# Kernel optimization log

Hardware: AMD Instinct MI355X
Metric: run time of the kernel (lower is better)

Reference implementation:

```python
import jax, jax.numpy as jnp
import numpy as np
import math

B, N, M, O = 64, 2048, 64, 128  # batch, neurons, in_dims, out_dims


def setup_inputs() -> dict:
    key = jax.random.key(0)
    kx, kw, kb = jax.random.split(key, 3)
    s = 1.0 / math.sqrt(M + O)
    x = jax.random.normal(kx, (B, N, M), dtype=jnp.float32)
    # master weights fp32, init U(-s, s) as in the torch module
    w1 = jax.random.uniform(kw, (M, O, N), dtype=jnp.float32, minval=-s, maxval=s)
    b1 = jnp.zeros((1, N, O), dtype=jnp.float32)
    return {"x": x, "w1": w1, "b1": b1}


def reference(x, w1, b1):
    # N independent per-neuron linears: [B,N,M] x [M,O,N] -> [B,N,O]
    # cast master weights/bias to compute dtype (matches .to(x.dtype))
    w = w1.astype(x.dtype)
    b = b1.astype(x.dtype)
    return jnp.einsum('bnm,mon->bno', x, w) + b
```

## Files before the change

### kernel.cpp

```cpp
#include <hip/hip_runtime.h>
#include <hip/hip_bf16.h>

#define N_TOT 2048
#define M_DIM 64
#define O_DIM 128
#define NT 8

typedef __bf16 bf16x8 __attribute__((ext_vector_type(8)));
typedef float f32x4 __attribute__((ext_vector_type(4)));

__global__ __launch_bounds__(512, 2) void superlinear_mfma(
    const float* __restrict__ x, const float* __restrict__ w1,
    const float* __restrict__ b1, float* __restrict__ out)
{
    __shared__ unsigned char wlds[3 * NT * 32 * M_DIM * 2];

    const int tid  = threadIdx.x;
    const int lane = tid & 63;
    const int wave = tid >> 6;

    const int bid  = blockIdx.x;
    const int nblk = (bid & 7) * 32 + (bid >> 3);
    const int n0   = nblk * NT;
    const int n    = n0 + wave;

    const int col = lane & 15;
    const int kg  = lane >> 4;

    const int half = tid & 1;
    const int ol   = (tid >> 1) & 31;
    const int mseg = tid >> 6;

    const size_t MSTR = (size_t)O_DIM * N_TOT;

    auto stage_issue = [&](int c, float4* r) {
        const float* gp = w1 + ((size_t)(mseg * 8) * O_DIM + (c * 32 + ol)) * N_TOT
                             + n0 + half * 4;
        #pragma unroll
        for (int mm = 0; mm < 8; ++mm)
            r[mm] = *(const float4*)(gp + (size_t)mm * MSTR);
    };
    auto stage_write = [&](int c, const float4* r) {
        unsigned base = (unsigned)(c % 3) * 32768u;
        #pragma unroll
        for (int j = 0; j < 4; ++j) {
            int nn = half * 4 + j;
            bf16x8 v;
            #pragma unroll
            for (int mm = 0; mm < 8; ++mm)
                v[mm] = (__bf16)(((const float*)&r[mm])[j]);
            unsigned addr = (unsigned)(nn * 4096 + ol * 128 + mseg * 16);
            addr ^= (unsigned)((ol & 7) << 4);
            *(bf16x8*)(wlds + base + addr) = v;
        }
    };

    float4 srA[8], srB[8];
    stage_issue(0, srA);

    float4 xr[2][4][2];
    #pragma unroll
    for (int kc = 0; kc < 2; ++kc)
        #pragma unroll
        for (int bt = 0; bt < 4; ++bt) {
            int b = bt * 16 + col;
            const float* xp = x + ((size_t)b * N_TOT + n) * M_DIM + kc * 32 + kg * 8;
            xr[kc][bt][0] = *(const float4*)xp;
            xr[kc][bt][1] = *(const float4*)(xp + 4);
        }
    float bv[8];
    #pragma unroll
    for (int ot = 0; ot < 8; ++ot)
        bv[ot] = b1[(size_t)n * O_DIM + ot * 16 + col];

    stage_issue(1, srB);

    stage_write(0, srA);

    bf16x8 af[2][4];
    #pragma unroll
    for (int kc = 0; kc < 2; ++kc)
        #pragma unroll
        for (int bt = 0; bt < 4; ++bt) {
            const float* lp = (const float*)&xr[kc][bt][0];
            const float* hp = (const float*)&xr[kc][bt][1];
            bf16x8 v;
            #pragma unroll
            for (int j = 0; j < 4; ++j) {
                v[j]     = (__bf16)lp[j];
                v[4 + j] = (__bf16)hp[j];
            }
            af[kc][bt] = v;
        }

    asm volatile("s_waitcnt lgkmcnt(0)" ::: "memory");
    __builtin_amdgcn_s_barrier();
    __builtin_amdgcn_sched_barrier(0);

    const unsigned sw = (unsigned)(col & 7) << 4;
    #pragma unroll
    for (int c = 0; c < 4; ++c) {
        if (c < 2) stage_issue(c + 2, (c & 1) ? srB : srA);

        unsigned base = (unsigned)(c % 3) * 32768u;
        f32x4 acc[4][2];
        #pragma unroll
        for (int otl = 0; otl < 2; ++otl) {
            unsigned la = (unsigned)(wave * 4096 + otl * 2048 + col * 128 + kg * 16);
            bf16x8 bf0 = *(const bf16x8*)(wlds + base + (la ^ sw));
            bf16x8 bf1 = *(const bf16x8*)(wlds + base + ((la + 64) ^ sw));
            f32x4 ci;
            float b0 = bv[c * 2 + otl];
            ci[0] = b0; ci[1] = b0; ci[2] = b0; ci[3] = b0;
            #pragma unroll
            for (int bt = 0; bt < 4; ++bt) {
                acc[bt][otl] = __builtin_amdgcn_mfma_f32_16x16x32_bf16(af[0][bt], bf0, ci,           0, 0, 0);
                acc[bt][otl] = __builtin_amdgcn_mfma_f32_16x16x32_bf16(af[1][bt], bf1, acc[bt][otl], 0, 0, 0);
            }
        }

        if (c < 3) stage_write(c + 1, (c & 1) ? srA : srB);

        #pragma unroll
        for (int bt = 0; bt < 4; ++bt)
            #pragma unroll
            for (int r = 0; r < 4; ++r) {
                int b = bt * 16 + kg * 4 + r;
                float* op = out + ((size_t)b * N_TOT + n) * O_DIM + c * 32 + col;
                op[0]  = acc[bt][0][r];
                op[16] = acc[bt][1][r];
            }

        if (c < 3) {
            asm volatile("s_waitcnt lgkmcnt(0)" ::: "memory");
            __builtin_amdgcn_s_barrier();
            __builtin_amdgcn_sched_barrier(0);
        }
    }
}

extern "C" void kernel_launch(void* const* d_in, const int* in_sizes, int n_in,
                              void* d_out, int out_size, void* d_ws, size_t ws_size,
                              hipStream_t stream) {
    const float* x  = (const float*)d_in[0];
    const float* w1 = (const float*)d_in[1];
    const float* b1 = (const float*)d_in[2];
    float* out = (float*)d_out;
    superlinear_mfma<<<dim3(256), dim3(512), 0, stream>>>(x, w1, b1, out);
}
```

Before: 35.42 us.

## Split output dim across blocks; use 1024 smaller blocks with single-stage LDS

Restructures the grid so each block handles 8 neurons and a 32-wide slice of the output dimension, launching 1024 blocks of 256 threads instead of 256 blocks of 512. The weight slice is staged into LDS once, which removes the triple-buffered per-chunk pipeline and the barriers inside the loop. Each wave now covers two neurons and iterates over batch tiles, prefetching the next x tile while it computes. The aim is more blocks for occupancy and load balance and less synchronisation, at the cost of re-reading x four times (once per output slice) and losing the overlap of weight loads with compute.

```diff
diff --git a/kernel.cpp b/kernel.cpp
--- a/kernel.cpp
+++ b/kernel.cpp
@@ -5,24 +5,27 @@
 #define M_DIM 64
 #define O_DIM 128
 #define NT 8
+#define OC 32
 
 typedef __bf16 bf16x8 __attribute__((ext_vector_type(8)));
 typedef float f32x4 __attribute__((ext_vector_type(4)));
 
-__global__ __launch_bounds__(512, 2) void superlinear_mfma(
+__global__ __launch_bounds__(256, 4) void superlinear_mfma(
     const float* __restrict__ x, const float* __restrict__ w1,
     const float* __restrict__ b1, float* __restrict__ out)
 {
-    __shared__ unsigned char wlds[3 * NT * 32 * M_DIM * 2];
+    __shared__ unsigned char wlds[NT * OC * M_DIM * 2];
 
     const int tid  = threadIdx.x;
     const int lane = tid & 63;
     const int wave = tid >> 6;
 
-    const int bid  = blockIdx.x;
-    const int nblk = (bid & 7) * 32 + (bid >> 3);
-    const int n0   = nblk * NT;
-    const int n    = n0 + wave;
+    const int bid = blockIdx.x;
+    const int swz = (bid & 7) * 128 + (bid >> 3);
+    const int nq  = swz >> 2;
+    const int oq  = swz & 3;
+    const int n0  = nq * NT;
+    const int o0  = oq * OC;
 
     const int col = lane & 15;
     const int kg  = lane >> 4;
@@ -33,108 +36,97 @@
 
     const size_t MSTR = (size_t)O_DIM * N_TOT;
 
-    auto stage_issue = [&](int c, float4* r) {
-        const float* gp = w1 + ((size_t)(mseg * 8) * O_DIM + (c * 32 + ol)) * N_TOT
+    float4 sr[16];
+    {
+        const float* gp = w1 + ((size_t)(mseg * 16) * O_DIM + (o0 + ol)) * N_TOT
                              + n0 + half * 4;
         #pragma unroll
-        for (int mm = 0; mm < 8; ++mm)
-            r[mm] = *(const float4*)(gp + (size_t)mm * MSTR);
+        for (int mm = 0; mm < 16; ++mm)
+            sr[mm] = *(const float4*)(gp + (size_t)mm * MSTR);
+    }
+
+    float bv[2][2];
+    #pragma unroll
+    for (int n2 = 0; n2 < 2; ++n2)
+        #pragma unroll
+        for (int ot = 0; ot < 2; ++ot)
+            bv[n2][ot] = b1[(size_t)(n0 + wave * 2 + n2) * O_DIM + o0 + ot * 16 + col];
+
+    float4 xr[8];
+    auto load_x = [&](int bt, float4* r) {
+        #pragma unroll
+        for (int n2 = 0; n2 < 2; ++n2)
+            #pragma unroll
+            for (int kc = 0; kc < 2; ++kc) {
+                const float* xp = x
+                    + ((size_t)(bt * 16 + col) * N_TOT + (n0 + wave * 2 + n2)) * M_DIM
+                    + kc * 32 + kg * 8;
+                r[n2 * 4 + kc * 2 + 0] = *(const float4*)xp;
+                r[n2 * 4 + kc * 2 + 1] = *(const float4*)(xp + 4);
+            }
     };
-    auto stage_write = [&](int c, const float4* r) {
-        unsigned base = (unsigned)(c % 3) * 32768u;
+    load_x(0, xr);
+
+    #pragma unroll
+    for (int j = 0; j < 4; ++j) {
+        int nn = half * 4 + j;
         #pragma unroll
-        for (int j = 0; j < 4; ++j) {
-            int nn = half * 4 + j;
+        for (int q = 0; q < 2; ++q) {
             bf16x8 v;
             #pragma unroll
-            for (int mm = 0; mm < 8; ++mm)
-                v[mm] = (__bf16)(((const float*)&r[mm])[j]);
-            unsigned addr = (unsigned)(nn * 4096 + ol * 128 + mseg * 16);
+            for (int t = 0; t < 8; ++t)
+                v[t] = (__bf16)(((const float*)&sr[q * 8 + t])[j]);
+            unsigned addr = (unsigned)(nn * 4096 + ol * 128 + mseg * 32 + q * 16);
             addr ^= (unsigned)((ol & 7) << 4);
-            *(bf16x8*)(wlds + base + addr) = v;
+            *(bf16x8*)(wlds + addr) = v;
         }
-    };
+    }
 
-    float4 srA[8], srB[8];
-    stage_issue(0, srA);
-
-    float4 xr[2][4][2];
-    #pragma unroll
-    for (int kc = 0; kc < 2; ++kc)
-        #pragma unroll
-        for (int bt = 0; bt < 4; ++bt) {
-            int b = bt * 16 + col;
-            const float* xp = x + ((size_t)b * N_TOT + n) * M_DIM + kc * 32 + kg * 8;
-            xr[kc][bt][0] = *(const float4*)xp;
-            xr[kc][bt][1] = *(const float4*)(xp + 4);
-        }
-    float bv[8];
-    #pragma unroll
-    for (int ot = 0; ot < 8; ++ot)
-        bv[ot] = b1[(size_t)n * O_DIM + ot * 16 + col];
-
-    stage_issue(1, srB);
-
-    stage_write(0, srA);
-
-    bf16x8 af[2][4];
-    #pragma unroll
-    for (int kc = 0; kc < 2; ++kc)
-        #pragma unroll
-        for (int bt = 0; bt < 4; ++bt) {
-            const float* lp = (const float*)&xr[kc][bt][0];
-            const float* hp = (const float*)&xr[kc][bt][1];
-            bf16x8 v;
-            #pragma unroll
-            for (int j = 0; j < 4; ++j) {
-                v[j]     = (__bf16)lp[j];
-                v[4 + j] = (__bf16)hp[j];
-            }
-            af[kc][bt] = v;
-        }
-
-    asm volatile("s_waitcnt lgkmcnt(0)" ::: "memory");
-    __builtin_amdgcn_s_barrier();
-    __builtin_amdgcn_sched_barrier(0);
+    __syncthreads();
 
     const unsigned sw = (unsigned)(col & 7) << 4;
     #pragma unroll
-    for (int c = 0; c < 4; ++c) {
-        if (c < 2) stage_issue(c + 2, (c & 1) ? srB : srA);
-
-        unsigned base = (unsigned)(c % 3) * 32768u;
-        f32x4 acc[4][2];
+    for (int bt = 0; bt < 4; ++bt) {
+        bf16x8 af[2][2];
         #pragma unroll
-        for (int otl = 0; otl < 2; ++otl) {
-            unsigned la = (unsigned)(wave * 4096 + otl * 2048 + col * 128 + kg * 16);
-            bf16x8 bf0 = *(const bf16x8*)(wlds + base + (la ^ sw));
-            bf16x8 bf1 = *(const bf16x8*)(wlds + base + ((la + 64) ^ sw));
-            f32x4 ci;
-            float b0 = bv[c * 2 + otl];
-            ci[0] = b0; ci[1] = b0; ci[2] = b0; ci[3] = b0;
+        for (int n2 = 0; n2 < 2; ++n2)
             #pragma unroll
-            for (int bt = 0; bt < 4; ++bt) {
-                acc[bt][otl] = __builtin_amdgcn_mfma_f32_16x16x32_bf16(af[0][bt], bf0, ci,           0, 0, 0);
-                acc[bt][otl] = __builtin_amdgcn_mfma_f32_16x16x32_bf16(af[1][bt], bf1, acc[bt][otl], 0, 0, 0);
+            for (int kc = 0; kc < 2; ++kc) {
+                const float* lp = (const float*)&xr[n2 * 4 + kc * 2 + 0];
+                const float* hp = (const float*)&xr[n2 * 4 + kc * 2 + 1];
+                bf16x8 v;
+                #pragma unroll
+                for (int t = 0; t < 4; ++t) {
+                    v[t]     = (__bf16)lp[t];
+                    v[4 + t] = (__bf16)hp[t];
+                }
+                af[n2][kc] = v;
             }
-        }
-
-        if (c < 3) stage_write(c + 1, (c & 1) ? srA : srB);
+        if (bt < 3) load_x(bt + 1, xr);
 
         #pragma unroll
-        for (int bt = 0; bt < 4; ++bt)
+        for (int n2 = 0; n2 < 2; ++n2) {
+            int nn = wave * 2 + n2;
+            int n  = n0 + nn;
+            f32x4 aa[2];
+            #pragma unroll
+            for (int ot = 0; ot < 2; ++ot) {
+                unsigned la = (unsigned)(nn * 4096 + (ot * 16 + col) * 128 + kg * 16);
+                bf16x8 bf0 = *(const bf16x8*)(wlds + (la ^ sw));
+                bf16x8 bf1 = *(const bf16x8*)(wlds + ((la + 64) ^ sw));
+                f32x4 ci;
+                float b0 = bv[n2][ot];
+                ci[0] = b0; ci[1] = b0; ci[2] = b0; ci[3] = b0;
+                aa[ot] = __builtin_amdgcn_mfma_f32_16x16x32_bf16(af[n2][0], bf0, ci,     0, 0, 0);
+                aa[ot] = __builtin_amdgcn_mfma_f32_16x16x32_bf16(af[n2][1], bf1, aa[ot], 0, 0, 0);
+            }
             #pragma unroll
             for (int r = 0; r < 4; ++r) {
                 int b = bt * 16 + kg * 4 + r;
-                float* op = out + ((size_t)b * N_TOT + n) * O_DIM + c * 32 + col;
-                op[0]  = acc[bt][0][r];
-                op[16] = acc[bt][1][r];
+                float* op = out + ((size_t)b * N_TOT + n) * O_DIM + o0 + col;
+                op[0]  = aa[0][r];
+                op[16] = aa[1][r];
             }
-
-        if (c < 3) {
-            asm volatile("s_waitcnt lgkmcnt(0)" ::: "memory");
-            __builtin_amdgcn_s_barrier();
-            __builtin_amdgcn_sched_barrier(0);
         }
     }
 }
@@ -146,5 +138,5 @@
     const float* w1 = (const float*)d_in[1];
     const float* b1 = (const float*)d_in[2];
     float* out = (float*)d_out;
-    superlinear_mfma<<<dim3(256), dim3(512), 0, stream>>>(x, w1, b1, out);
+    superlinear_mfma<<<dim3(1024), dim3(256), 0, stream>>>(x, w1, b1, out);
 }
```

Result: slower. 36.28 us (+2.4%).

## Retile blocks to 16 neurons by half of output dims, two neurons per wave

Applied to the files above, without the earlier changes.

Each block now covers 16 neurons and a 64-wide output half instead of 8 neurons and all 128 outputs. Each wave handles two neurons, and weight staging chunks shrink to 16 output columns per stage. Results from consecutive chunks are held back so stores are written as paired 32-column groups. This changes the per-thread weight load pattern (64-byte contiguous rows across 16 neurons) and the reuse balance between x and weights. In exchange, x is loaded twice, once per output half, and register pressure rises from the doubled x fragments and the saved accumulators.

```diff
diff --git a/kernel.cpp b/kernel.cpp
--- a/kernel.cpp
+++ b/kernel.cpp
@@ -4,7 +4,8 @@
 #define N_TOT 2048
 #define M_DIM 64
 #define O_DIM 128
-#define NT 8
+#define NT 16
+#define OC 64
 
 typedef __bf16 bf16x8 __attribute__((ext_vector_type(8)));
 typedef float f32x4 __attribute__((ext_vector_type(4)));
@@ -13,29 +14,31 @@
     const float* __restrict__ x, const float* __restrict__ w1,
     const float* __restrict__ b1, float* __restrict__ out)
 {
-    __shared__ unsigned char wlds[3 * NT * 32 * M_DIM * 2];
+    __shared__ unsigned char wlds[3 * 32768];
 
     const int tid  = threadIdx.x;
     const int lane = tid & 63;
     const int wave = tid >> 6;
 
     const int bid  = blockIdx.x;
-    const int nblk = (bid & 7) * 32 + (bid >> 3);
-    const int n0   = nblk * NT;
-    const int n    = n0 + wave;
+    const int swz  = (bid & 7) * 32 + (bid >> 3);
+    const int ngrp = swz >> 1;
+    const int oh   = swz & 1;
+    const int n0   = ngrp * NT;
+    const int o0   = oh * OC;
 
     const int col = lane & 15;
     const int kg  = lane >> 4;
 
-    const int half = tid & 1;
-    const int ol   = (tid >> 1) & 31;
+    const int q    = tid & 3;
+    const int ol   = (tid >> 2) & 15;
     const int mseg = tid >> 6;
 
     const size_t MSTR = (size_t)O_DIM * N_TOT;
 
     auto stage_issue = [&](int c, float4* r) {
-        const float* gp = w1 + ((size_t)(mseg * 8) * O_DIM + (c * 32 + ol)) * N_TOT
-                             + n0 + half * 4;
+        const float* gp = w1 + ((size_t)(mseg * 8) * O_DIM + (o0 + c * 16 + ol)) * N_TOT
+                             + n0 + q * 4;
         #pragma unroll
         for (int mm = 0; mm < 8; ++mm)
             r[mm] = *(const float4*)(gp + (size_t)mm * MSTR);
@@ -44,12 +47,12 @@
         unsigned base = (unsigned)(c % 3) * 32768u;
         #pragma unroll
         for (int j = 0; j < 4; ++j) {
-            int nn = half * 4 + j;
+            int nn = q * 4 + j;
             bf16x8 v;
             #pragma unroll
             for (int mm = 0; mm < 8; ++mm)
                 v[mm] = (__bf16)(((const float*)&r[mm])[j]);
-            unsigned addr = (unsigned)(nn * 4096 + ol * 128 + mseg * 16);
+            unsigned addr = (unsigned)(nn * 2048 + ol * 128 + mseg * 16);
             addr ^= (unsigned)((ol & 7) << 4);
             *(bf16x8*)(wlds + base + addr) = v;
         }
@@ -58,78 +61,100 @@
     float4 srA[8], srB[8];
     stage_issue(0, srA);
 
-    float4 xr[2][4][2];
+    float4 xr[2][4][4];
     #pragma unroll
-    for (int kc = 0; kc < 2; ++kc)
+    for (int n2 = 0; n2 < 2; ++n2)
         #pragma unroll
         for (int bt = 0; bt < 4; ++bt) {
             int b = bt * 16 + col;
-            const float* xp = x + ((size_t)b * N_TOT + n) * M_DIM + kc * 32 + kg * 8;
-            xr[kc][bt][0] = *(const float4*)xp;
-            xr[kc][bt][1] = *(const float4*)(xp + 4);
+            int n = n0 + wave * 2 + n2;
+            const float* xp = x + ((size_t)b * N_TOT + n) * M_DIM + kg * 8;
+            xr[n2][bt][0] = *(const float4*)xp;
+            xr[n2][bt][1] = *(const float4*)(xp + 4);
+            xr[n2][bt][2] = *(const float4*)(xp + 32);
+            xr[n2][bt][3] = *(const float4*)(xp + 36);
         }
-    float bv[8];
+    float bv[2][4];
     #pragma unroll
-    for (int ot = 0; ot < 8; ++ot)
-        bv[ot] = b1[(size_t)n * O_DIM + ot * 16 + col];
+    for (int n2 = 0; n2 < 2; ++n2)
+        #pragma unroll
+        for (int c = 0; c < 4; ++c)
+            bv[n2][c] = b1[(size_t)(n0 + wave * 2 + n2) * O_DIM + o0 + c * 16 + col];
 
     stage_issue(1, srB);
 
     stage_write(0, srA);
 
-    bf16x8 af[2][4];
+    bf16x8 af[2][2][4];
     #pragma unroll
-    for (int kc = 0; kc < 2; ++kc)
+    for (int n2 = 0; n2 < 2; ++n2)
         #pragma unroll
-        for (int bt = 0; bt < 4; ++bt) {
-            const float* lp = (const float*)&xr[kc][bt][0];
-            const float* hp = (const float*)&xr[kc][bt][1];
-            bf16x8 v;
+        for (int kc = 0; kc < 2; ++kc)
             #pragma unroll
-            for (int j = 0; j < 4; ++j) {
-                v[j]     = (__bf16)lp[j];
-                v[4 + j] = (__bf16)hp[j];
+            for (int bt = 0; bt < 4; ++bt) {
+                const float* lp = (const float*)&xr[n2][bt][kc * 2 + 0];
+                const float* hp = (const float*)&xr[n2][bt][kc * 2 + 1];
+                bf16x8 v;
+                #pragma unroll
+                for (int t = 0; t < 4; ++t) {
+                    v[t]     = (__bf16)lp[t];
+                    v[4 + t] = (__bf16)hp[t];
+                }
+                af[n2][kc][bt] = v;
             }
-            af[kc][bt] = v;
-        }
 
     asm volatile("s_waitcnt lgkmcnt(0)" ::: "memory");
     __builtin_amdgcn_s_barrier();
     __builtin_amdgcn_sched_barrier(0);
 
     const unsigned sw = (unsigned)(col & 7) << 4;
+    f32x4 accP[2][4];
     #pragma unroll
     for (int c = 0; c < 4; ++c) {
         if (c < 2) stage_issue(c + 2, (c & 1) ? srB : srA);
 
         unsigned base = (unsigned)(c % 3) * 32768u;
-        f32x4 acc[4][2];
+        f32x4 acc[2][4];
         #pragma unroll
-        for (int otl = 0; otl < 2; ++otl) {
-            unsigned la = (unsigned)(wave * 4096 + otl * 2048 + col * 128 + kg * 16);
+        for (int n2 = 0; n2 < 2; ++n2) {
+            int nn = wave * 2 + n2;
+            unsigned la = (unsigned)(nn * 2048 + col * 128 + kg * 16);
             bf16x8 bf0 = *(const bf16x8*)(wlds + base + (la ^ sw));
             bf16x8 bf1 = *(const bf16x8*)(wlds + base + ((la + 64) ^ sw));
             f32x4 ci;
-            float b0 = bv[c * 2 + otl];
+            float b0 = bv[n2][c];
             ci[0] = b0; ci[1] = b0; ci[2] = b0; ci[3] = b0;
             #pragma unroll
             for (int bt = 0; bt < 4; ++bt) {
-                acc[bt][otl] = __builtin_amdgcn_mfma_f32_16x16x32_bf16(af[0][bt], bf0, ci,           0, 0, 0);
-                acc[bt][otl] = __builtin_amdgcn_mfma_f32_16x16x32_bf16(af[1][bt], bf1, acc[bt][otl], 0, 0, 0);
+                acc[n2][bt] = __builtin_amdgcn_mfma_f32_16x16x32_bf16(af[n2][0][bt], bf0, ci,          0, 0, 0);
+                acc[n2][bt] = __builtin_amdgcn_mfma_f32_16x16x32_bf16(af[n2][1][bt], bf1, acc[n2][bt], 0, 0, 0);
             }
         }
 
         if (c < 3) stage_write(c + 1, (c & 1) ? srA : srB);
 
-        #pragma unroll
-        for (int bt = 0; bt < 4; ++bt)
+        if (c & 1) {
             #pragma unroll
-            for (int r = 0; r < 4; ++r) {
-                int b = bt * 16 + kg * 4 + r;
-                float* op = out + ((size_t)b * N_TOT + n) * O_DIM + c * 32 + col;
-                op[0]  = acc[bt][0][r];
-                op[16] = acc[bt][1][r];
+            for (int n2 = 0; n2 < 2; ++n2) {
+                int n = n0 + wave * 2 + n2;
+                #pragma unroll
+                for (int bt = 0; bt < 4; ++bt)
+                    #pragma unroll
+                    for (int r = 0; r < 4; ++r) {
+                        int b = bt * 16 + kg * 4 + r;
+                        float* op = out + ((size_t)b * N_TOT + n) * O_DIM
+                                        + o0 + (c - 1) * 16 + col;
+                        op[0]  = accP[n2][bt][r];
+                        op[16] = acc[n2][bt][r];
+                    }
             }
+        } else {
+            #pragma unroll
+            for (int n2 = 0; n2 < 2; ++n2)
+                #pragma unroll
+                for (int bt = 0; bt < 4; ++bt)
+                    accP[n2][bt] = acc[n2][bt];
+        }
 
         if (c < 3) {
             asm volatile("s_waitcnt lgkmcnt(0)" ::: "memory");
```

Result: no change. 35.77 us (+1.0%).
